# Optimization experiments

Hardware: AMD Instinct MI355X
Metric: run time of the kernel (lower is better)

The kernel has to match this reference:

```python
import jax, jax.numpy as jnp
import numpy as np

ANCHOR = 12.0      # anchor (d,h,w) size used for parametrization
NMS_IOU = 0.25     # suppression threshold
TOPK = 2048        # pre-NMS candidate cap (= stop_after), fixed for jit


def setup_inputs() -> dict:
    key = jax.random.key(0)
    k1, k2 = jax.random.split(key)
    bboxes = jax.random.normal(k1, (2, 6, 64, 96, 96), dtype=jnp.float32)
    scores = jax.random.normal(k2, (2, 64, 96, 96), dtype=jnp.float32)
    return {"bboxes": bboxes, "scores": scores}


def _deparametrize(bboxes):
    # bboxes: (B, 6, D, H, W), parametrized as in Ren et al. 2017
    D, H, W = bboxes.shape[2:]
    axes = [jnp.arange(s, dtype=bboxes.dtype) + 0.5 for s in (D, H, W)]
    zyx = jnp.stack(jnp.meshgrid(*axes, indexing='ij'))        # (3, D, H, W)
    abs_zyx = bboxes[:, :3] * ANCHOR + zyx[None]               # center coords
    abs_dhw = jnp.exp(bboxes[:, 3:]) * ANCHOR                  # sizes
    return jnp.concatenate([abs_zyx, abs_dhw], axis=1)


def _pairwise_iou(b1, b2):
    # b1: (N,6), b2: (M,6) with (z,y,x,d,h,w)
    c1, s1 = b1[:, :3], b1[:, 3:]
    c2, s2 = b2[:, :3], b2[:, 3:]
    lo = jnp.maximum((c1 - s1 / 2)[:, None, :], (c2 - s2 / 2)[None, :, :])
    hi = jnp.minimum((c1 + s1 / 2)[:, None, :], (c2 + s2 / 2)[None, :, :])
    inter = jnp.clip(hi - lo, 0).prod(-1)                      # (N, M)
    union = s1.prod(-1)[:, None] + s2.prod(-1)[None, :] - inter
    return inter / union


def _nms_one(boxes_flat, scores_flat):
    # boxes_flat: (P, 6), scores_flat: (P,)
    scores_top, idx = jax.lax.top_k(scores_flat, TOPK)
    boxes_top = boxes_flat[idx]                                # (K, 6)
    ious = _pairwise_iou(boxes_top, boxes_top)                 # (K, K)
    ar = jnp.arange(TOPK)

    def body(keep, i):
        # suppress lower-scored boxes overlapping a kept box i
        suppress = (ious[i] > NMS_IOU) & (ar > i) & keep[i]
        return keep & ~suppress, None

    keep, _ = jax.lax.scan(body, jnp.ones(TOPK, dtype=bool), ar)
    out = jnp.concatenate([scores_top[:, None], boxes_top], axis=1)  # (K, 7)
    return jnp.where(keep[:, None], out, 0.0)


def reference(bboxes, scores):
    abs_boxes = _deparametrize(bboxes)                         # (B, 6, D, H, W)
    B = bboxes.shape[0]
    boxes_flat = abs_boxes.reshape(B, 6, -1).transpose(0, 2, 1)  # (B, P, 6)
    scores_flat = scores.reshape(B, -1)                          # (B, P)
    # (B, TOPK, 7): column 0 = score, columns 1:7 = (z,y,x,d,h,w); suppressed rows zeroed
    return jax.vmap(_nms_one)(boxes_flat, scores_flat)
```

## Files before the change

kernel.cpp:

```cpp
#include <hip/hip_runtime.h>
#include <math.h>

typedef unsigned int U32;
typedef unsigned long long U64;

constexpr int N_SP   = 64 * 96 * 96;
constexpr int NBATCH = 2;
constexpr int K_TOP  = 2048;
constexpr int NBINS  = 8192;
constexpr int CAP    = 8192;
constexpr int CAPB   = 64;
constexpr float ANCHOR_F = 12.0f;
constexpr float NMS_IOU_F = 0.25f;

constexpr size_t OFF_HIST = 0;
constexpr size_t OFF_CNT  = OFF_HIST + 2 * NBINS * 4;
constexpr size_t OFF_CAND = OFF_CNT + 256;
constexpr size_t OFF_BOX  = OFF_CAND + 2 * CAP * 8;
constexpr size_t OFF_MASK = OFF_BOX + 2 * 14 * K_TOP * 4;
constexpr size_t OFF_DIAG = OFF_MASK + 2 * K_TOP * 64 * 4;
constexpr size_t OFF_BCNT = OFF_DIAG + 2 * K_TOP * 4;
constexpr size_t OFF_BKT  = OFF_BCNT + 512;

__device__ __forceinline__ U32 mono_of(float f) {
  U32 u = __float_as_uint(f);
  return (u & 0x80000000u) ? ~u : (u | 0x80000000u);
}
__device__ __forceinline__ float un_mono(U32 m) {
  U32 u = (m & 0x80000000u) ? (m ^ 0x80000000u) : ~m;
  return __uint_as_float(u);
}

__global__ void __launch_bounds__(256) k_zero(U32* hist, U32* cnt, U32* bcnt) {
  int g = blockIdx.x * 256 + threadIdx.x;
  hist[g] = 0;
  if (g < NBATCH) cnt[g] = 0;
  if (g < 2 * 64) bcnt[g] = 0;
}

__global__ void __launch_bounds__(256) k_hist(const float* __restrict__ scores,
                                              U32* __restrict__ hist) {
  int b = blockIdx.y;
  const float4* s4 = (const float4*)(scores + (size_t)b * N_SP)
                     + (size_t)blockIdx.x * 2048 + threadIdx.x;
  float4 v[8];
#pragma unroll
  for (int e = 0; e < 8; ++e) v[e] = s4[e * 256];
  __shared__ U32 lh[NBINS];
  for (int k = threadIdx.x; k < NBINS; k += 256) lh[k] = 0;
  __syncthreads();
#pragma unroll
  for (int e = 0; e < 8; ++e) {
    atomicAdd(&lh[mono_of(v[e].x) >> 19], 1u);
    atomicAdd(&lh[mono_of(v[e].y) >> 19], 1u);
    atomicAdd(&lh[mono_of(v[e].z) >> 19], 1u);
    atomicAdd(&lh[mono_of(v[e].w) >> 19], 1u);
  }
  __syncthreads();
  U32* gh = hist + (size_t)b * NBINS;
  for (int k = threadIdx.x; k < NBINS; k += 256) {
    U32 c = lh[k];
    if (c) atomicAdd(&gh[k], c);
  }
}

__global__ void __launch_bounds__(256) k_collect(const float* __restrict__ scores,
                                                 const U32* __restrict__ hist,
                                                 U32* __restrict__ cnt,
                                                 U64* __restrict__ cand) {
  int b = blockIdx.y;
  int tid = threadIdx.x;
  const float4* s4 = (const float4*)(scores + (size_t)b * N_SP)
                     + (size_t)blockIdx.x * 1024 + tid;
  float4 v[4];
#pragma unroll
  for (int e = 0; e < 4; ++e) v[e] = s4[e * 256];

  __shared__ U32 part[256];
  __shared__ U32 sthr;
  const U32* h = hist + (size_t)b * NBINS;
  {
    int base = NBINS - 32 * (tid + 1);
    U32 s = 0;
    for (int k = 0; k < 32; ++k) s += h[base + k];
    part[tid] = s;
  }
  __syncthreads();
  if (tid == 0) {
    U32 cum = 0, bin = 0;
    for (int c = 0; c < 256; ++c) {
      U32 p = part[c];
      if (cum + p >= (U32)K_TOP) {
        int hb = NBINS - 32 * c - 1;
        for (int k = 0; k < 32; ++k) {
          cum += h[hb - k];
          if (cum >= (U32)K_TOP) { bin = (U32)(hb - k); break; }
        }
        break;
      }
      cum += p;
    }
    sthr = bin;
  }
  __syncthreads();
  U32 tb = sthr;

  __shared__ U64 lbuf[4096];
  __shared__ U32 lcnt, lbase;
  if (tid == 0) lcnt = 0;
  __syncthreads();
#pragma unroll
  for (int e = 0; e < 4; ++e) {
    U32 i0 = (blockIdx.x * 1024 + e * 256 + tid) * 4;
    float vv[4] = {v[e].x, v[e].y, v[e].z, v[e].w};
#pragma unroll
    for (int c = 0; c < 4; ++c) {
      U32 m = mono_of(vv[c]);
      if ((m >> 19) >= tb) {
        U32 p = atomicAdd(&lcnt, 1u);
        lbuf[p] = ((U64)m << 32) | (U32)(~(i0 + c));
      }
    }
  }
  __syncthreads();
  if (tid == 0 && lcnt) lbase = atomicAdd(&cnt[b], lcnt);
  __syncthreads();
  U32 n = lcnt;
  if (n == 0) return;
  U32 base = lbase;
  U64* cb = cand + (size_t)b * CAP;
  for (U32 k = tid; k < n; k += 256) {
    U32 pos = base + k;
    if (pos < (U32)CAP) cb[pos] = lbuf[k];
  }
}

#pragma clang fp contract(off)

__global__ void __launch_bounds__(256) k_cg(const float* __restrict__ bboxes,
                                            const U64* __restrict__ cand,
                                            const U32* __restrict__ cnt,
                                            float* __restrict__ box) {
  int b = blockIdx.y;
  int tid = threadIdx.x;
  U32 C = cnt[b]; if (C > (U32)CAP) C = CAP;
  if ((U32)(blockIdx.x * 256) >= C) return;
  const U64* cb = cand + (size_t)b * CAP;
  __shared__ U64 s[CAP];
  for (U32 k = tid; k < C; k += 256) s[k] = cb[k];
  __syncthreads();
  U32 t = (U32)(blockIdx.x * 256 + tid);
  U64 kv = (t < C) ? s[t] : 0ull;
  U32 rk = 0;
#pragma unroll 16
  for (U32 j = 0; j < C; ++j) rk += (s[j] > kv) ? 1u : 0u;
  if (t >= C || rk >= (U32)K_TOP) return;
  U32 r = rk;
  U64 key = kv;
  U32 idx = ~(U32)(key & 0xFFFFFFFFull);
  float sc = un_mono((U32)(key >> 32));
  int d = idx / 9216;
  int rem = idx - d * 9216;
  int h = rem / 96;
  int w = rem - h * 96;
  const float* src = bboxes + (size_t)b * 6 * N_SP + idx;
  float r0 = src[0];
  float r1 = src[(size_t)N_SP];
  float r2 = src[(size_t)2 * N_SP];
  float r3 = src[(size_t)3 * N_SP];
  float r4 = src[(size_t)4 * N_SP];
  float r5 = src[(size_t)5 * N_SP];
  float cz = r0 * ANCHOR_F + ((float)d + 0.5f);
  float cy = r1 * ANCHOR_F + ((float)h + 0.5f);
  float cx = r2 * ANCHOR_F + ((float)w + 0.5f);
  float sz = (float)exp((double)r3) * ANCHOR_F;
  float sy = (float)exp((double)r4) * ANCHOR_F;
  float sx = (float)exp((double)r5) * ANCHOR_F;
  float* B0 = box + (size_t)b * 14 * K_TOP;
  B0[0 * K_TOP + r] = cz;  B0[1 * K_TOP + r] = cy;  B0[2 * K_TOP + r] = cx;
  B0[3 * K_TOP + r] = sz;  B0[4 * K_TOP + r] = sy;  B0[5 * K_TOP + r] = sx;
  B0[6 * K_TOP + r] = cz - sz * 0.5f;
  B0[7 * K_TOP + r] = cy - sy * 0.5f;
  B0[8 * K_TOP + r] = cx - sx * 0.5f;
  B0[9 * K_TOP + r] = cz + sz * 0.5f;
  B0[10 * K_TOP + r] = cy + sy * 0.5f;
  B0[11 * K_TOP + r] = cx + sx * 0.5f;
  B0[12 * K_TOP + r] = (sz * sy) * sx;
  B0[13 * K_TOP + r] = sc;
}

__global__ void __launch_bounds__(256) k_mask(const float* __restrict__ box,
                                              U32* __restrict__ mask,
                                              U32* __restrict__ diag,
                                              U32* __restrict__ bcnt,
                                              U64* __restrict__ bkt) {
  int b = blockIdx.y;
  int it = blockIdx.x >> 2;
  int jq = blockIdx.x & 3;
  const float* B0 = box + (size_t)b * 14 * K_TOP;
  __shared__ float ls[7][512];
  int j0 = jq * 512;
  for (int k = threadIdx.x; k < 7 * 512; k += 256) {
    int a = k >> 9, j = k & 511;
    ls[a][j] = B0[(size_t)(6 + a) * K_TOP + j0 + j];
  }
  __syncthreads();
  int lane = threadIdx.x & 63;
  int wv = threadIdx.x >> 6;
  int i = it * 64 + lane;
  float imin0 = B0[6 * K_TOP + i], imin1 = B0[7 * K_TOP + i], imin2 = B0[8 * K_TOP + i];
  float imax0 = B0[9 * K_TOP + i], imax1 = B0[10 * K_TOP + i], imax2 = B0[11 * K_TOP + i];
  float ivol  = B0[12 * K_TOP + i];
  U32 wbits[4];
  int jb = wv * 128;
#pragma unroll
  for (int wl = 0; wl < 4; ++wl) {
    U32 bits = 0;
    for (int bit = 0; bit < 32; ++bit) {
      int jl = jb + wl * 32 + bit;
      int j = j0 + jl;
      float lo0 = fmaxf(imin0, ls[0][jl]);
      float lo1 = fmaxf(imin1, ls[1][jl]);
      float lo2 = fmaxf(imin2, ls[2][jl]);
      float hi0 = fminf(imax0, ls[3][jl]);
      float hi1 = fminf(imax1, ls[4][jl]);
      float hi2 = fminf(imax2, ls[5][jl]);
      float d0 = fmaxf(hi0 - lo0, 0.0f);
      float d1 = fmaxf(hi1 - lo1, 0.0f);
      float d2 = fmaxf(hi2 - lo2, 0.0f);
      float inter = (d0 * d1) * d2;
      float uni = (ivol + ls[6][jl]) - inter;
      float iou = inter / uni;
      bits |= ((iou > NMS_IOU_F) && (j > i)) ? (1u << bit) : 0u;
    }
    wbits[wl] = bits;
  }
  uint4* mrow = (uint4*)(mask + ((size_t)(b * K_TOP + i)) * 64);
  mrow[jq * 4 + wv] = make_uint4(wbits[0], wbits[1], wbits[2], wbits[3]);
  U32* dgp = diag + (size_t)b * K_TOP;
  int g_src = i >> 5;
  U32* bc = bcnt + b * 64 + g_src;
  U64* bb = bkt + ((size_t)(b * 64 + g_src)) * CAPB;
#pragma unroll
  for (int wl = 0; wl < 4; ++wl) {
    int w = jq * 16 + wv * 4 + wl;
    if (w == (i >> 5)) dgp[i] = wbits[wl];
    if (wbits[wl]) {
      U32 p = atomicAdd(bc, 1u);
      if (p < (U32)CAPB)
        bb[p] = ((U64)((U32)((i & 31) << 6) | (U32)w) << 32) | wbits[wl];
    }
  }
}

__global__ void __launch_bounds__(256) k_nms(const float* __restrict__ box,
                                             const U32* __restrict__ mask,
                                             const U32* __restrict__ diag,
                                             const U32* __restrict__ bcnt,
                                             const U64* __restrict__ bkt,
                                             float* __restrict__ out) {
  int b = blockIdx.x;
  int tid = threadIdx.x;
  int wv = tid >> 6, lane = tid & 63;
  const U32* mk = mask + (size_t)b * K_TOP * 64;
  const U32* dgp = diag + (size_t)b * K_TOP;
  const U32* bcg = bcnt + b * 64;
  const U64* bkg = bkt + (size_t)b * 64 * CAPB;

  __shared__ U64 lbkt[64 * CAPB];
  __shared__ U32 ldiag[K_TOP];
  __shared__ U32 lcnt[64];
  __shared__ U32 keepArr[64];

  for (int k = tid; k < K_TOP; k += 256) ldiag[k] = dgp[k];
  for (int k = tid; k < 64 * CAPB; k += 256) lbkt[k] = bkg[k];
  if (tid < 64) lcnt[tid] = bcg[tid];
  __syncthreads();

  if (wv == 0) {
    U32 keep = 0xFFFFFFFFu;
    U32 cnt_l = lcnt[lane];
    bool ovf = (__ballot(cnt_l > (U32)CAPB) != 0ull);
    if (!ovf) {
      for (int g = 0; g < 64; ++g) {
        U32 kw = (U32)__builtin_amdgcn_readlane((int)keep, g);
        if (!kw) continue;
        U32 dgl = ldiag[g * 32 + (lane & 31)];
        U32 nzw = (U32)__ballot(dgl != 0);
        U32 m = kw & nzw;
        while (m) {
          int q = __builtin_ctz(m);
          if ((kw >> q) & 1u)
            kw &= ~(U32)__builtin_amdgcn_readlane((int)dgl, q);
          m &= m - 1;
        }
        U32 n = (U32)__builtin_amdgcn_readlane((int)cnt_l, g);
        U32 acc = 0;
        for (U32 e0 = 0; e0 < n; e0 += 64) {
          U64 ev = lbkt[(U32)g * CAPB + e0 + (U32)lane];
          U32 evLo = (U32)ev, evHi = (U32)(ev >> 32);
          U32 lim = (n - e0 > 64u) ? 64u : (n - e0);
          for (U32 t = 0; t < lim; ++t) {
            U32 hi = (U32)__builtin_amdgcn_readlane((int)evHi, (int)t);
            U32 bt = (U32)__builtin_amdgcn_readlane((int)evLo, (int)t);
            U32 il = (hi >> 6) & 31u, w = hi & 63u;
            if ((kw >> il) & 1u)
              acc |= (w == (U32)lane) ? bt : 0u;
          }
        }
        keep &= ~acc;
      }
    } else {
      for (int g = 0; g < 64; ++g) {
        U32 kw = (U32)__builtin_amdgcn_readlane((int)keep, g);
        U32 dgl = ldiag[g * 32 + (lane & 31)];
#pragma unroll
        for (int q = 0; q < 32; ++q)
          if ((kw >> q) & 1u)
            kw &= ~(U32)__builtin_amdgcn_readlane((int)dgl, q);
        U32 rw[32];
#pragma unroll
        for (int q = 0; q < 32; ++q)
          rw[q] = mk[(size_t)(g * 32 + q) * 64 + lane];
        U32 acc = 0;
#pragma unroll
        for (int q = 0; q < 32; ++q) acc |= ((kw >> q) & 1u) ? rw[q] : 0u;
        keep &= ~acc;
      }
    }
    keepArr[lane] = keep;
  }
  __syncthreads();

  const float* B0 = box + (size_t)b * 14 * K_TOP;
  for (int t = tid; t < K_TOP; t += 256) {
    U32 kp = (keepArr[t >> 5] >> (t & 31)) & 1u;
    float sc = B0[13 * K_TOP + t];
    float vz = B0[0 * K_TOP + t], vy = B0[1 * K_TOP + t], vx = B0[2 * K_TOP + t];
    float dz = B0[3 * K_TOP + t], dy = B0[4 * K_TOP + t], dx = B0[5 * K_TOP + t];
    float* o = out + (size_t)(b * K_TOP + t) * 7;
    o[0] = kp ? sc : 0.0f;
    o[1] = kp ? vz : 0.0f;
    o[2] = kp ? vy : 0.0f;
    o[3] = kp ? vx : 0.0f;
    o[4] = kp ? dz : 0.0f;
    o[5] = kp ? dy : 0.0f;
    o[6] = kp ? dx : 0.0f;
  }
}

extern "C" void kernel_launch(void* const* d_in, const int* in_sizes, int n_in,
                              void* d_out, int out_size, void* d_ws, size_t ws_size,
                              hipStream_t stream) {
  const float* bboxes = (const float*)d_in[0];
  const float* scores = (const float*)d_in[1];
  float* out = (float*)d_out;

  char* ws = (char*)d_ws;
  U32* hist = (U32*)(ws + OFF_HIST);
  U32* cnt  = (U32*)(ws + OFF_CNT);
  U64* cand = (U64*)(ws + OFF_CAND);
  float* box = (float*)(ws + OFF_BOX);
  U32* mask = (U32*)(ws + OFF_MASK);
  U32* diag = (U32*)(ws + OFF_DIAG);
  U32* bcnt = (U32*)(ws + OFF_BCNT);
  U64* bkt  = (U64*)(ws + OFF_BKT);

  k_zero<<<64, 256, 0, stream>>>(hist, cnt, bcnt);
  k_hist<<<dim3(72, NBATCH), 256, 0, stream>>>(scores, hist);
  k_collect<<<dim3(144, NBATCH), 256, 0, stream>>>(scores, hist, cnt, cand);
  k_cg<<<dim3(32, NBATCH), 256, 0, stream>>>(bboxes, cand, cnt, box);
  k_mask<<<dim3(128, NBATCH), 256, 0, stream>>>(box, mask, diag, bcnt, bkt);
  k_nms<<<NBATCH, 256, 0, stream>>>(box, mask, diag, bcnt, bkt, out);
}
```

Measured before the change: 175.8 us.

## Split candidate rank counting into segmented parallel kernel with atomic accumulation

The rank computation for top-K candidates used to run inside the gather kernel, where each of 32 blocks per batch loaded all candidates into shared memory and looped over every one of them. It is now a separate kernel that splits the comparison range into 8 segments over 256 blocks per batch and sums partial counts into a global rank array with atomics. The gather kernel then just reads the rank. This spreads the quadratic work across many more CUs, at the cost of an extra launch, global-memory reads in place of LDS, and atomics.

```diff
diff --git a/kernel.cpp b/kernel.cpp
--- a/kernel.cpp
+++ b/kernel.cpp
@@ -21,6 +21,7 @@
 constexpr size_t OFF_DIAG = OFF_MASK + 2 * K_TOP * 64 * 4;
 constexpr size_t OFF_BCNT = OFF_DIAG + 2 * K_TOP * 4;
 constexpr size_t OFF_BKT  = OFF_BCNT + 512;
+constexpr size_t OFF_RANK = OFF_BKT + 2 * 64 * CAPB * 8;
 
 __device__ __forceinline__ U32 mono_of(float f) {
   U32 u = __float_as_uint(f);
@@ -31,9 +32,11 @@
   return __uint_as_float(u);
 }
 
-__global__ void __launch_bounds__(256) k_zero(U32* hist, U32* cnt, U32* bcnt) {
+__global__ void __launch_bounds__(256) k_zero(U32* hist, U32* rank, U32* cnt,
+                                              U32* bcnt) {
   int g = blockIdx.x * 256 + threadIdx.x;
   hist[g] = 0;
+  rank[g] = 0;
   if (g < NBATCH) cnt[g] = 0;
   if (g < 2 * 64) bcnt[g] = 0;
 }
@@ -135,28 +138,39 @@
   }
 }
 
+__global__ void __launch_bounds__(256) k_count(const U64* __restrict__ cand,
+                                               const U32* __restrict__ cnt,
+                                               U32* __restrict__ rank) {
+  int b = blockIdx.y;
+  U32 C = cnt[b]; if (C > (U32)CAP) C = CAP;
+  U32 g = blockIdx.x * 256 + threadIdx.x;
+  U32 t = g & (CAP - 1);
+  U32 sgm = g >> 13;
+  if (t >= C) return;
+  const U64* cb = cand + (size_t)b * CAP;
+  U64 key = cb[t];
+  U32 segLen = (C + 7) >> 3;
+  U32 j0 = sgm * segLen;
+  U32 j1 = j0 + segLen; if (j1 > C) j1 = C;
+  U32 c = 0;
+  for (U32 j = j0; j < j1; ++j) c += (cb[j] > key) ? 1u : 0u;
+  if (c) atomicAdd(&rank[(size_t)b * CAP + t], c);
+}
+
 #pragma clang fp contract(off)
 
-__global__ void __launch_bounds__(256) k_cg(const float* __restrict__ bboxes,
-                                            const U64* __restrict__ cand,
-                                            const U32* __restrict__ cnt,
-                                            float* __restrict__ box) {
-  int b = blockIdx.y;
-  int tid = threadIdx.x;
+__global__ void __launch_bounds__(256) k_gather(const float* __restrict__ bboxes,
+                                                const U64* __restrict__ cand,
+                                                const U32* __restrict__ cnt,
+                                                const U32* __restrict__ rank,
+                                                float* __restrict__ box) {
+  int b = blockIdx.y;
   U32 C = cnt[b]; if (C > (U32)CAP) C = CAP;
-  if ((U32)(blockIdx.x * 256) >= C) return;
-  const U64* cb = cand + (size_t)b * CAP;
-  __shared__ U64 s[CAP];
-  for (U32 k = tid; k < C; k += 256) s[k] = cb[k];
-  __syncthreads();
-  U32 t = (U32)(blockIdx.x * 256 + tid);
-  U64 kv = (t < C) ? s[t] : 0ull;
-  U32 rk = 0;
-#pragma unroll 16
-  for (U32 j = 0; j < C; ++j) rk += (s[j] > kv) ? 1u : 0u;
-  if (t >= C || rk >= (U32)K_TOP) return;
-  U32 r = rk;
-  U64 key = kv;
+  U32 t = blockIdx.x * 256 + threadIdx.x;
+  if (t >= C) return;
+  U32 r = rank[(size_t)b * CAP + t];
+  if (r >= (U32)K_TOP) return;
+  U64 key = cand[(size_t)b * CAP + t];
   U32 idx = ~(U32)(key & 0xFFFFFFFFull);
   float sc = un_mono((U32)(key >> 32));
   int d = idx / 9216;
@@ -365,11 +379,13 @@
   U32* diag = (U32*)(ws + OFF_DIAG);
   U32* bcnt = (U32*)(ws + OFF_BCNT);
   U64* bkt  = (U64*)(ws + OFF_BKT);
-
-  k_zero<<<64, 256, 0, stream>>>(hist, cnt, bcnt);
+  U32* rank = (U32*)(ws + OFF_RANK);
+
+  k_zero<<<64, 256, 0, stream>>>(hist, rank, cnt, bcnt);
   k_hist<<<dim3(72, NBATCH), 256, 0, stream>>>(scores, hist);
   k_collect<<<dim3(144, NBATCH), 256, 0, stream>>>(scores, hist, cnt, cand);
-  k_cg<<<dim3(32, NBATCH), 256, 0, stream>>>(bboxes, cand, cnt, box);
+  k_count<<<dim3(256, NBATCH), 256, 0, stream>>>(cand, cnt, rank);
+  k_gather<<<dim3(CAP / 256, NBATCH), 256, 0, stream>>>(bboxes, cand, cnt, rank, box);
   k_mask<<<dim3(128, NBATCH), 256, 0, stream>>>(box, mask, diag, bcnt, bkt);
   k_nms<<<NBATCH, 256, 0, stream>>>(box, mask, diag, bcnt, bkt, out);
 }
```

After: 181.8 us. +3.4%, slower.
